# Kernel tuning notes

Measured on AMD Instinct MI355X. Metric: run time of the kernel, lower is better.

Reference implementation:

```python
import jax, jax.numpy as jnp
import numpy as np

N_NODES = 50000
N_EDGES = 800000
D_IN = 256
HID = 128
OUT = 64
NEG_SLOPE = 0.2  # PyG GATConv default leaky_relu slope
EPS = 1e-16      # PyG softmax denominator epsilon


def _gat_conv(x, src, dst, W_src, W_dst, att_src, att_dst, bias, n_nodes):
    """Single-head PyG GATConv with add_self_loops=False.
    Returns (out [N, C_out], alpha [E])."""
    h_src = x @ W_src                     # [N, C]
    h_dst = x @ W_dst                     # [N, C]
    a_src = h_src @ att_src               # [N]
    a_dst = h_dst @ att_dst               # [N]
    logits = jax.nn.leaky_relu(a_src[src] + a_dst[dst], NEG_SLOPE)  # [E]
    # segment softmax over incoming edges of each dst node
    m = jax.ops.segment_max(logits, dst, num_segments=n_nodes)      # [N]
    e = jnp.exp(logits - m[dst])                                    # [E]
    denom = jax.ops.segment_sum(e, dst, num_segments=n_nodes)       # [N]
    alpha = e / (denom[dst] + EPS)                                  # [E]
    msg = h_src[src] * alpha[:, None]                               # [E, C]
    out = jax.ops.segment_sum(msg, dst, num_segments=n_nodes) + bias
    return out, alpha


def setup_inputs() -> dict:
    key = jax.random.key(0)
    ks = jax.random.split(key, 16)
    s = 0.05
    x = jax.random.normal(ks[0], (N_NODES, D_IN), dtype=jnp.float32)
    edge_index = jax.random.randint(ks[1], (2, N_EDGES), 0, N_NODES, dtype=jnp.int64)
    return {
        "x": x,
        "edge_index": edge_index,
        "W_src1": jax.random.normal(ks[2], (D_IN, HID), jnp.float32) * s,
        "W_dst1": jax.random.normal(ks[3], (D_IN, HID), jnp.float32) * s,
        "att_src1": jax.random.normal(ks[4], (HID,), jnp.float32) * s,
        "att_dst1": jax.random.normal(ks[5], (HID,), jnp.float32) * s,
        "b1": jnp.zeros((HID,), jnp.float32),
        "W_lin1": jax.random.normal(ks[6], (D_IN, HID), jnp.float32) * s,
        "b_lin1": jnp.zeros((HID,), jnp.float32),
        "W_src2": jax.random.normal(ks[7], (HID, OUT), jnp.float32) * s,
        "W_dst2": jax.random.normal(ks[8], (HID, OUT), jnp.float32) * s,
        "att_src2": jax.random.normal(ks[9], (OUT,), jnp.float32) * s,
        "att_dst2": jax.random.normal(ks[10], (OUT,), jnp.float32) * s,
        "b2": jnp.zeros((OUT,), jnp.float32),
        "W_lin2": jax.random.normal(ks[11], (HID, OUT), jnp.float32) * s,
        "b_lin2": jnp.zeros((OUT,), jnp.float32),
    }


def reference(x, edge_index, W_src1, W_dst1, att_src1, att_dst1, b1, W_lin1, b_lin1,
              W_src2, W_dst2, att_src2, att_dst2, b2, W_lin2, b_lin2):
    src, dst = edge_index[0], edge_index[1]
    n = x.shape[0]
    h, _ = _gat_conv(x, src, dst, W_src1, W_dst1, att_src1, att_dst1, b1, n)
    h = h + x @ W_lin1 + b_lin1
    h = jax.nn.relu(h)
    out, alpha = _gat_conv(h, src, dst, W_src2, W_dst2, att_src2, att_dst2, b2, n)
    out = out + h @ W_lin2 + b_lin2
    return out, alpha
```

## Files before the change

### kernel.cpp

```cpp
#include <hip/hip_runtime.h>
#include <math.h>

#define D_IN 256
#define HID 128
#define D_OUT 64
#define NEG_SLOPE 0.2f

#define NBUCK 196
#define BCAP  5120
#define P1_EPB 8192

typedef short short8 __attribute__((ext_vector_type(8)));
typedef float floatx4 __attribute__((ext_vector_type(4)));

__device__ __forceinline__ float wave_reduce_sum(float v) {
    #pragma unroll
    for (int off = 32; off > 0; off >>= 1) v += __shfl_xor(v, off, 64);
    return v;
}
__device__ __forceinline__ int wave_scan_incl_i(int v) {
    int lane = threadIdx.x & 63;
    #pragma unroll
    for (int off = 1; off < 64; off <<= 1) {
        int t = __shfl_up(v, off, 64);
        if (lane >= off) v += t;
    }
    return v;
}

__device__ __forceinline__ short f2bf(float f) {
    unsigned u = __float_as_uint(f);
    u += 0x7fffu + ((u >> 16) & 1u);
    return (short)(u >> 16);
}
__device__ __forceinline__ unsigned pk2(float a, float b) {
    return (unsigned)(unsigned short)f2bf(a) | ((unsigned)(unsigned short)f2bf(b) << 16);
}
__device__ __forceinline__ float bflo(unsigned p) { return __uint_as_float(p << 16); }
__device__ __forceinline__ float bfhi(unsigned p) { return __uint_as_float(p & 0xffff0000u); }

__device__ void prep_body(const float* Wsrc1, const float* att_src1,
                          const float* Wdst1, const float* att_dst1,
                          const float* Wsrc2, const float* att_src2,
                          const float* Wdst2, const float* att_dst2,
                          const float* b1, const float* b_lin1,
                          const float* b2, const float* b_lin2,
                          float* v_src1, float* v_dst1, float* v_src2, float* v_dst2,
                          float* bsum1, float* bsum2) {
    int t = threadIdx.x;
    if (t < D_IN) {
        float s1 = 0.f, s2 = 0.f;
        for (int c = 0; c < HID; c++) {
            s1 += Wsrc1[t * HID + c] * att_src1[c];
            s2 += Wdst1[t * HID + c] * att_dst1[c];
        }
        v_src1[t] = s1; v_dst1[t] = s2;
    }
    if (t < HID) {
        float s1 = 0.f, s2 = 0.f;
        for (int c = 0; c < D_OUT; c++) {
            s1 += Wsrc2[t * D_OUT + c] * att_src2[c];
            s2 += Wdst2[t * D_OUT + c] * att_dst2[c];
        }
        v_src2[t] = s1; v_dst2[t] = s2;
        bsum1[t] = b1[t] + b_lin1[t];
    }
    if (t < D_OUT) bsum2[t] = b2[t] + b_lin2[t];
}

__device__ void pack_body(const float* Wa, const float* Wb, short* Wp,
                          int NTG, int NH, int total, int idx) {
    if (idx >= total) return;
    int j = idx & 7;
    int lane = (idx >> 3) & 63;
    int r = idx >> 9;
    int nt = r % NTG;
    int s = r / NTG;
    int k = s * 32 + ((lane >> 4) * 8) + j;
    int cg = nt * 16 + (lane & 15);
    const float* W = (cg < NH) ? Wa : Wb;
    int col = (cg < NH) ? cg : cg - NH;
    Wp[idx] = f2bf(W[(size_t)k * NH + col]);
}

__device__ void bucket_scatter_body(const int* __restrict__ src, const int* __restrict__ dst,
                                    int E, int* bcur, unsigned* ebuf, int blk) {
    __shared__ int hist[NBUCK];
    __shared__ int gbase[NBUCK];
    int t = threadIdx.x;
    for (int i = t; i < NBUCK; i += 256) hist[i] = 0;
    __syncthreads();
    int e0 = blk * P1_EPB;
    int e1 = e0 + P1_EPB; if (e1 > E) e1 = E;
    for (int e = e0 + t; e < e1; e += 256)
        atomicAdd(&hist[dst[e] >> 8], 1);
    __syncthreads();
    for (int i = t; i < NBUCK; i += 256) {
        gbase[i] = atomicAdd(&bcur[i], hist[i]);
        hist[i] = 0;
    }
    __syncthreads();
    for (int e = e0 + t; e < e1; e += 256) {
        int d = dst[e];
        int b = d >> 8;
        int slot = atomicAdd(&hist[b], 1);
        int pos = gbase[b] + slot;
        if (pos < BCAP)
            ebuf[(size_t)b * BCAP + pos] = (unsigned)src[e] | ((unsigned)(d & 255) << 16);
    }
}

__device__ void convert_body(const float* __restrict__ X, unsigned short* __restrict__ xb,
                             int Nn, int rb) {
    int row = rb * 4 + (threadIdx.x >> 6);
    int lane = threadIdx.x & 63;
    if (row >= Nn) return;
    float4 v = *(const float4*)(X + (size_t)row * D_IN + lane * 4);
    ushort4 o;
    o.x = (unsigned short)f2bf(v.x); o.y = (unsigned short)f2bf(v.y);
    o.z = (unsigned short)f2bf(v.z); o.w = (unsigned short)f2bf(v.w);
    *(ushort4*)(xb + (size_t)row * D_IN + lane * 4) = o;
}

__global__ void fused_pre(const int* __restrict__ src, const int* __restrict__ dst, int E,
                          int* bcur, unsigned* ebuf, int P1B,
                          const float* W_src1, const float* W_lin1, short* Wp1,
                          const float* W_src2, const float* W_lin2, short* Wp2,
                          const float* att_src1, const float* W_dst1, const float* att_dst1,
                          const float* att_src2, const float* W_dst2, const float* att_dst2,
                          const float* b1, const float* b_lin1,
                          const float* b2, const float* b_lin2,
                          float* v_src1, float* v_dst1, float* v_src2, float* v_dst2,
                          float* bsum1, float* bsum2,
                          const float* __restrict__ X, unsigned short* __restrict__ xb, int Nn) {
    int bid = blockIdx.x;
    if (bid < P1B) {
        bucket_scatter_body(src, dst, E, bcur, ebuf, bid);
    } else if (bid < P1B + 256) {
        pack_body(W_src1, W_lin1, Wp1, 16, HID, 8 * 16 * 512, (bid - P1B) * 256 + threadIdx.x);
    } else if (bid < P1B + 320) {
        pack_body(W_src2, W_lin2, Wp2, 8, D_OUT, 4 * 8 * 512, (bid - P1B - 256) * 256 + threadIdx.x);
    } else if (bid < P1B + 321) {
        prep_body(W_src1, att_src1, W_dst1, att_dst1, W_src2, att_src2, W_dst2, att_dst2,
                  b1, b_lin1, b2, b_lin2, v_src1, v_dst1, v_src2, v_dst2, bsum1, bsum2);
    } else {
        convert_body(X, xb, Nn, bid - (P1B + 321));
    }
}

__device__ void build_csr_body(const int* __restrict__ bcur, const unsigned* __restrict__ ebuf,
                               int* __restrict__ ssrc, int* __restrict__ row_beg,
                               int* __restrict__ row_end, int Nn, int b) {
    __shared__ int cnt[256];
    __shared__ int ofs[256];
    __shared__ int wsum[4];
    int t = threadIdx.x;
    cnt[t] = 0;
    __syncthreads();
    int n = bcur[b]; if (n > BCAP) n = BCAP;
    const unsigned* eb = ebuf + (size_t)b * BCAP;
    for (int i = t; i < n; i += 256)
        atomicAdd(&cnt[eb[i] >> 16], 1);
    __syncthreads();
    int v = cnt[t];
    int incl = wave_scan_incl_i(v);
    if ((t & 63) == 63) wsum[t >> 6] = incl;
    __syncthreads();
    int add = 0;
    #pragma unroll
    for (int w = 0; w < 4; w++) if (w < (t >> 6)) add += wsum[w];
    int excl = add + incl - v;
    int base = b * BCAP;
    int node = b * 256 + t;
    if (node < Nn) { row_beg[node] = base + excl; row_end[node] = base + excl + v; }
    ofs[t] = base + excl;
    __syncthreads();
    for (int i = t; i < n; i += 256) {
        unsigned r = eb[i];
        int pos = atomicAdd(&ofs[r >> 16], 1);
        ssrc[pos] = (int)(r & 0xffffu);
    }
}

__device__ void dots_body(const unsigned short* __restrict__ xb,
                          const float* __restrict__ vsrc, const float* __restrict__ vdst,
                          float* __restrict__ a_src, float* __restrict__ a_dst,
                          int Nn, int rb) {
    int row = rb * 4 + (threadIdx.x >> 6);
    int lane = threadIdx.x & 63;
    if (row >= Nn) return;
    uint2 p = *(const uint2*)(xb + (size_t)row * D_IN + lane * 4);
    float4 vs = *(const float4*)(vsrc + lane * 4);
    float4 vd = *(const float4*)(vdst + lane * 4);
    float x0 = bflo(p.x), x1 = bfhi(p.x), x2 = bflo(p.y), x3 = bfhi(p.y);
    float ps = x0 * vs.x + x1 * vs.y + x2 * vs.z + x3 * vs.w;
    float pd = x0 * vd.x + x1 * vd.y + x2 * vd.z + x3 * vd.w;
    ps = wave_reduce_sum(ps);
    pd = wave_reduce_sum(pd);
    if (lane == 0) { a_src[row] = ps; a_dst[row] = pd; }
}

template <int KS, int NT>
__device__ void gemm_body(const unsigned short* __restrict__ A,
                          const short* __restrict__ Wp,
                          const float* __restrict__ bias,
                          unsigned short* __restrict__ outb,
                          unsigned short* __restrict__ outc, int M, int bm) {
    const int K = KS * 32;
    const int NTG = 4 * NT;
    const int NH = NT * 32;
    int tid = threadIdx.x;
    int wave = tid >> 6, lane = tid & 63;
    int mr = lane & 15, quad = lane >> 4;

    floatx4 acc[4][NT];
    #pragma unroll
    for (int i = 0; i < 4; i++)
        #pragma unroll
        for (int j = 0; j < NT; j++) acc[i][j] = (floatx4){0.f, 0.f, 0.f, 0.f};

    const unsigned short* arow[4];
    #pragma unroll
    for (int tm = 0; tm < 4; tm++) {
        int gr = bm + tm * 16 + mr;
        if (gr >= M) gr = M - 1;
        arow[tm] = A + (size_t)gr * K + quad * 8;
    }
    const short* bbase = Wp + ((size_t)(wave * NT) * 64 + lane) * 8;

    #pragma unroll
    for (int s = 0; s < KS; s++) {
        short8 af[4], bf[NT];
        #pragma unroll
        for (int tm = 0; tm < 4; tm++)
            af[tm] = *(const short8*)(arow[tm] + s * 32);
        #pragma unroll
        for (int tn = 0; tn < NT; tn++)
            bf[tn] = *(const short8*)(bbase + ((size_t)s * NTG + tn) * 512);
        #pragma unroll
        for (int tn = 0; tn < NT; tn++)
            #pragma unroll
            for (int tm = 0; tm < 4; tm++)
                acc[tm][tn] = __builtin_amdgcn_mfma_f32_16x16x32_bf16(af[tm], bf[tn],
                                                                      acc[tm][tn], 0, 0, 0);
    }

    #pragma unroll
    for (int tm = 0; tm < 4; tm++) {
        #pragma unroll
        for (int tn = 0; tn < NT; tn++) {
            int cg = wave * NT * 16 + tn * 16 + mr;
            if (cg < NH) {
                #pragma unroll
                for (int r = 0; r < 4; r++) {
                    int gr = bm + tm * 16 + quad * 4 + r;
                    if (gr < M)
                        outb[(size_t)gr * NH + cg] = (unsigned short)f2bf(acc[tm][tn][r]);
                }
            } else {
                float bv = bias[cg - NH];
                #pragma unroll
                for (int r = 0; r < 4; r++) {
                    int gr = bm + tm * 16 + quad * 4 + r;
                    if (gr < M)
                        outc[(size_t)gr * NH + (cg - NH)] = (unsigned short)f2bf(acc[tm][tn][r] + bv);
                }
            }
        }
    }
}

__global__ __launch_bounds__(256, 3) void fused_g1(const unsigned short* __restrict__ xb,
                                                   const short* __restrict__ Wp1,
                                                   const float* __restrict__ bsum1,
                                                   unsigned short* __restrict__ h1b,
                                                   unsigned short* __restrict__ lin1b,
                                                   int M, int MB,
                                                   const int* __restrict__ bcur,
                                                   const unsigned* __restrict__ ebuf,
                                                   int* ssrc, int* row_beg, int* row_end, int Nn,
                                                   const float* __restrict__ v_src1,
                                                   const float* __restrict__ v_dst1,
                                                   float* a_src1, float* a_dst1) {
    int bid = blockIdx.x;
    if (bid < MB) {
        gemm_body<8, 4>(xb, Wp1, bsum1, h1b, lin1b, M, bid * 64);
    } else if (bid < MB + NBUCK) {
        build_csr_body(bcur, ebuf, ssrc, row_beg, row_end, Nn, bid - MB);
    } else {
        dots_body(xb, v_src1, v_dst1, a_src1, a_dst1, Nn, bid - MB - NBUCK);
    }
}

template <int KS, int NT>
__global__ __launch_bounds__(256, 3) void gemm_direct(const unsigned short* __restrict__ A,
                                                      const short* __restrict__ Wp,
                                                      const float* __restrict__ bias,
                                                      unsigned short* __restrict__ outb,
                                                      unsigned short* __restrict__ outc, int M) {
    gemm_body<KS, NT>(A, Wp, bias, outb, outc, M, blockIdx.x * 64);
}

__global__ void agg1_kernel(const int* __restrict__ row_beg, const int* __restrict__ row_end,
                            const int* __restrict__ ssrc,
                            const float* __restrict__ a_src, const float* __restrict__ a_dst,
                            const unsigned short* __restrict__ h1b,
                            const unsigned short* __restrict__ linb,
                            const float* __restrict__ vs2, const float* __restrict__ vd2,
                            unsigned short* __restrict__ hb,
                            float* __restrict__ a_src2, float* __restrict__ a_dst2, int Nn) {
    int node = blockIdx.x * 4 + (threadIdx.x >> 6);
    int lane = threadIdx.x & 63;
    if (node >= Nn) return;
    int beg = row_beg[node], end = row_end[node];
    float ad = a_dst[node];

    int qh = lane >> 4, cl = lane & 15;
    float acc[8] = {0.f, 0.f, 0.f, 0.f, 0.f, 0.f, 0.f, 0.f};
    float dsum = 0.f;
    const unsigned short* hcol = h1b + cl * 8;
    int j = beg + qh;
    for (; j + 4 < end; j += 8) {
        int s0 = ssrc[j], s1 = ssrc[j + 4];
        float l0 = a_src[s0] + ad; l0 = (l0 > 0.f) ? l0 : NEG_SLOPE * l0;
        float l1 = a_src[s1] + ad; l1 = (l1 > 0.f) ? l1 : NEG_SLOPE * l1;
        float w0 = __expf(l0), w1 = __expf(l1);
        uint4 p0 = *(const uint4*)(hcol + (size_t)s0 * HID);
        uint4 p1 = *(const uint4*)(hcol + (size_t)s1 * HID);
        acc[0] += w0 * bflo(p0.x); acc[1] += w0 * bfhi(p0.x);
        acc[2] += w0 * bflo(p0.y); acc[3] += w0 * bfhi(p0.y);
        acc[4] += w0 * bflo(p0.z); acc[5] += w0 * bfhi(p0.z);
        acc[6] += w0 * bflo(p0.w); acc[7] += w0 * bfhi(p0.w);
        acc[0] += w1 * bflo(p1.x); acc[1] += w1 * bfhi(p1.x);
        acc[2] += w1 * bflo(p1.y); acc[3] += w1 * bfhi(p1.y);
        acc[4] += w1 * bflo(p1.z); acc[5] += w1 * bfhi(p1.z);
        acc[6] += w1 * bflo(p1.w); acc[7] += w1 * bfhi(p1.w);
        if (cl == 0) dsum += w0 + w1;
    }
    for (; j < end; j += 4) {
        int s0 = ssrc[j];
        float l = a_src[s0] + ad; l = (l > 0.f) ? l : NEG_SLOPE * l;
        float w = __expf(l);
        uint4 p = *(const uint4*)(hcol + (size_t)s0 * HID);
        acc[0] += w * bflo(p.x); acc[1] += w * bfhi(p.x);
        acc[2] += w * bflo(p.y); acc[3] += w * bfhi(p.y);
        acc[4] += w * bflo(p.z); acc[5] += w * bfhi(p.z);
        acc[6] += w * bflo(p.w); acc[7] += w * bfhi(p.w);
        if (cl == 0) dsum += w;
    }
    #pragma unroll
    for (int i = 0; i < 8; i++) {
        acc[i] += __shfl_xor(acc[i], 16, 64);
        acc[i] += __shfl_xor(acc[i], 32, 64);
    }
    dsum = wave_reduce_sum(dsum);
    float inv = 1.f / (dsum + 1e-16f);

    int c = cl * 8;
    uint4 lb = *(const uint4*)(linb + (size_t)node * HID + c);
    float o[8];
    o[0] = fmaxf(acc[0] * inv + bflo(lb.x), 0.f);
    o[1] = fmaxf(acc[1] * inv + bfhi(lb.x), 0.f);
    o[2] = fmaxf(acc[2] * inv + bflo(lb.y), 0.f);
    o[3] = fmaxf(acc[3] * inv + bfhi(lb.y), 0.f);
    o[4] = fmaxf(acc[4] * inv + bflo(lb.z), 0.f);
    o[5] = fmaxf(acc[5] * inv + bfhi(lb.z), 0.f);
    o[6] = fmaxf(acc[6] * inv + bflo(lb.w), 0.f);
    o[7] = fmaxf(acc[7] * inv + bfhi(lb.w), 0.f);
    if (qh == 0) {
        uint4 pk;
        pk.x = pk2(o[0], o[1]); pk.y = pk2(o[2], o[3]);
        pk.z = pk2(o[4], o[5]); pk.w = pk2(o[6], o[7]);
        *(uint4*)&hb[(size_t)node * HID + c] = pk;
    }
    float ps = 0.f, pd = 0.f;
    #pragma unroll
    for (int i = 0; i < 8; i++) { ps += o[i] * vs2[c + i]; pd += o[i] * vd2[c + i]; }
    ps = wave_reduce_sum(ps) * 0.25f;
    pd = wave_reduce_sum(pd) * 0.25f;
    if (lane == 0) { a_src2[node] = ps; a_dst2[node] = pd; }
}

__global__ void agg2_kernel(const int* __restrict__ row_beg, const int* __restrict__ row_end,
                            const int* __restrict__ ssrc,
                            const float* __restrict__ a_src, const float* __restrict__ a_dst,
                            const unsigned short* __restrict__ h2b,
                            const unsigned short* __restrict__ lin2b,
                            float* __restrict__ out, float* __restrict__ sminv, int Nn) {
    int node = blockIdx.x * 4 + (threadIdx.x >> 6);
    int lane = threadIdx.x & 63;
    if (node >= Nn) return;
    int beg = row_beg[node], end = row_end[node];
    float ad = a_dst[node];

    int oh = lane >> 3, cl = lane & 7;
    float acc[8] = {0.f, 0.f, 0.f, 0.f, 0.f, 0.f, 0.f, 0.f};
    float dsum = 0.f;
    const unsigned short* hcol = h2b + cl * 8;
    int j = beg + oh;
    for (; j + 8 < end; j += 16) {
        int s0 = ssrc[j], s1 = ssrc[j + 8];
        float l0 = a_src[s0] + ad; l0 = (l0 > 0.f) ? l0 : NEG_SLOPE * l0;
        float l1 = a_src[s1] + ad; l1 = (l1 > 0.f) ? l1 : NEG_SLOPE * l1;
        float w0 = __expf(l0), w1 = __expf(l1);
        uint4 p0 = *(const uint4*)(hcol + (size_t)s0 * D_OUT);
        uint4 p1 = *(const uint4*)(hcol + (size_t)s1 * D_OUT);
        acc[0] += w0 * bflo(p0.x); acc[1] += w0 * bfhi(p0.x);
        acc[2] += w0 * bflo(p0.y); acc[3] += w0 * bfhi(p0.y);
        acc[4] += w0 * bflo(p0.z); acc[5] += w0 * bfhi(p0.z);
        acc[6] += w0 * bflo(p0.w); acc[7] += w0 * bfhi(p0.w);
        acc[0] += w1 * bflo(p1.x); acc[1] += w1 * bfhi(p1.x);
        acc[2] += w1 * bflo(p1.y); acc[3] += w1 * bfhi(p1.y);
        acc[4] += w1 * bflo(p1.z); acc[5] += w1 * bfhi(p1.z);
        acc[6] += w1 * bflo(p1.w); acc[7] += w1 * bfhi(p1.w);
        if (cl == 0) dsum += w0 + w1;
    }
    for (; j < end; j += 8) {
        int s0 = ssrc[j];
        float l = a_src[s0] + ad; l = (l > 0.f) ? l : NEG_SLOPE * l;
        float w = __expf(l);
        uint4 p = *(const uint4*)(hcol + (size_t)s0 * D_OUT);
        acc[0] += w * bflo(p.x); acc[1] += w * bfhi(p.x);
        acc[2] += w * bflo(p.y); acc[3] += w * bfhi(p.y);
        acc[4] += w * bflo(p.z); acc[5] += w * bfhi(p.z);
        acc[6] += w * bflo(p.w); acc[7] += w * bfhi(p.w);
        if (cl == 0) dsum += w;
    }
    #pragma unroll
    for (int i = 0; i < 8; i++) {
        acc[i] += __shfl_xor(acc[i], 8, 64);
        acc[i] += __shfl_xor(acc[i], 16, 64);
        acc[i] += __shfl_xor(acc[i], 32, 64);
    }
    dsum = wave_reduce_sum(dsum);
    float inv = 1.f / (dsum + 1e-16f);
    if (lane == 0) sminv[node] = inv;

    if (oh == 0) {
        int c = cl * 8;
        uint4 lb = *(const uint4*)(lin2b + (size_t)node * D_OUT + c);
        float4 oa = make_float4(acc[0] * inv + bflo(lb.x), acc[1] * inv + bfhi(lb.x),
                                acc[2] * inv + bflo(lb.y), acc[3] * inv + bfhi(lb.y));
        float4 ob = make_float4(acc[4] * inv + bflo(lb.z), acc[5] * inv + bfhi(lb.z),
                                acc[6] * inv + bflo(lb.w), acc[7] * inv + bfhi(lb.w));
        *(float4*)&out[(size_t)node * D_OUT + c] = oa;
        *(float4*)&out[(size_t)node * D_OUT + c + 4] = ob;
    }
}

__global__ void alpha_kernel(const int* __restrict__ src, const int* __restrict__ dst,
                             const float* __restrict__ a_src2, const float* __restrict__ a_dst2,
                             const float* __restrict__ sminv, float* __restrict__ alpha, int E) {
    int e = blockIdx.x * 256 + threadIdx.x;
    if (e >= E) return;
    int s = src[e], d = dst[e];
    float l = a_src2[s] + a_dst2[d];
    l = (l > 0.f) ? l : NEG_SLOPE * l;
    alpha[e] = __expf(l) * sminv[d];
}

extern "C" void kernel_launch(void* const* d_in, const int* in_sizes, int n_in,
                              void* d_out, int out_size, void* d_ws, size_t ws_size,
                              hipStream_t stream) {
    const float* x        = (const float*)d_in[0];
    const int*   ei       = (const int*)d_in[1];
    const float* W_src1   = (const float*)d_in[2];
    const float* W_dst1   = (const float*)d_in[3];
    const float* att_src1 = (const float*)d_in[4];
    const float* att_dst1 = (const float*)d_in[5];
    const float* b1       = (const float*)d_in[6];
    const float* W_lin1   = (const float*)d_in[7];
    const float* b_lin1   = (const float*)d_in[8];
    const float* W_src2   = (const float*)d_in[9];
    const float* W_dst2   = (const float*)d_in[10];
    const float* att_src2 = (const float*)d_in[11];
    const float* att_dst2 = (const float*)d_in[12];
    const float* b2       = (const float*)d_in[13];
    const float* W_lin2   = (const float*)d_in[14];
    const float* b_lin2   = (const float*)d_in[15];

    const int Nn = in_sizes[0] / D_IN;
    const int E  = in_sizes[1] / 2;
    const int* src = ei;
    const int* dst = ei + E;

    char* w = (char*)d_ws;
    auto alloc = [&](size_t bytes) { char* p = w; w += (bytes + 255) & ~(size_t)255; return p; };
    unsigned short* xb   = (unsigned short*)alloc((size_t)Nn * D_IN * 2);
    unsigned short* h1b  = (unsigned short*)alloc((size_t)Nn * HID * 2);
    unsigned short* lin1b= (unsigned short*)alloc((size_t)Nn * HID * 2);
    unsigned short* hb   = (unsigned short*)alloc((size_t)Nn * HID * 2);
    unsigned short* h2b  = (unsigned short*)alloc((size_t)Nn * D_OUT * 2);
    unsigned short* lin2b= (unsigned short*)alloc((size_t)Nn * D_OUT * 2);
    float* a_src1 = (float*)alloc((size_t)Nn * 4);
    float* a_dst1 = (float*)alloc((size_t)Nn * 4);
    float* a_src2 = (float*)alloc((size_t)Nn * 4);
    float* a_dst2 = (float*)alloc((size_t)Nn * 4);
    float* sminv  = (float*)alloc((size_t)Nn * 4);
    int*   row_beg= (int*)alloc((size_t)Nn * 4);
    int*   row_end= (int*)alloc((size_t)Nn * 4);
    int*   bcur   = (int*)alloc((size_t)NBUCK * 4);
    unsigned* ebuf= (unsigned*)alloc((size_t)NBUCK * BCAP * 4);
    int*   ssrc   = (int*)alloc((size_t)NBUCK * BCAP * 4);
    short* Wp1    = (short*)alloc((size_t)8 * 16 * 512 * 2);
    short* Wp2    = (short*)alloc((size_t)4 * 8 * 512 * 2);
    float* v_src1 = (float*)alloc(D_IN * 4);
    float* v_dst1 = (float*)alloc(D_IN * 4);
    float* v_src2 = (float*)alloc(HID * 4);
    float* v_dst2 = (float*)alloc(HID * 4);
    float* bsum1  = (float*)alloc(HID * 4);
    float* bsum2  = (float*)alloc(D_OUT * 4);

    float* out       = (float*)d_out;
    float* alpha_out = out + (size_t)Nn * D_OUT;

    hipMemsetAsync(bcur, 0, (size_t)NBUCK * 4, stream);

    int P1B = (E + P1_EPB - 1) / P1_EPB;
    int ablocks = (Nn + 3) / 4;
    fused_pre<<<P1B + 321 + ablocks, 256, 0, stream>>>(src, dst, E, bcur, ebuf, P1B,
                                             W_src1, W_lin1, Wp1, W_src2, W_lin2, Wp2,
                                             att_src1, W_dst1, att_dst1,
                                             att_src2, W_dst2, att_dst2,
                                             b1, b_lin1, b2, b_lin2,
                                             v_src1, v_dst1, v_src2, v_dst2, bsum1, bsum2,
                                             x, xb, Nn);

    int mblocks = (Nn + 63) / 64;
    fused_g1<<<mblocks + NBUCK + ablocks, 256, 0, stream>>>(xb, Wp1, bsum1, h1b, lin1b, Nn,
                                                            mblocks, bcur, ebuf, ssrc,
                                                            row_beg, row_end, Nn,
                                                            v_src1, v_dst1, a_src1, a_dst1);

    agg1_kernel<<<ablocks, 256, 0, stream>>>(row_beg, row_end, ssrc, a_src1, a_dst1, h1b, lin1b,
                                             v_src2, v_dst2, hb, a_src2, a_dst2, Nn);

    gemm_direct<4, 2><<<mblocks, 256, 0, stream>>>(hb, Wp2, bsum2, h2b, lin2b, Nn);
    agg2_kernel<<<ablocks, 256, 0, stream>>>(row_beg, row_end, ssrc, a_src2, a_dst2, h2b, lin2b,
                                             out, sminv, Nn);
    int eblocks = (E + 255) / 256;
    alpha_kernel<<<eblocks, 256, 0, stream>>>(src, dst, a_src2, a_dst2, sminv, alpha_out, E);
}
```

Baseline: 275.5 us.

## Split CSR build into finer sub-buckets interleaved with GEMM blocks

```diff
diff --git a/kernel.cpp b/kernel.cpp
--- a/kernel.cpp
+++ b/kernel.cpp
@@ -6,9 +6,11 @@
 #define D_OUT 64
 #define NEG_SLOPE 0.2f
 
-#define NBUCK 196
-#define BCAP  5120
-#define P1_EPB 8192
+#define NBUCK 392
+#define BCAP  2560
+#define NSUB  784
+#define SCAP  1280
+#define P1_EPB 2048
 
 typedef short short8 __attribute__((ext_vector_type(8)));
 typedef float floatx4 __attribute__((ext_vector_type(4)));
@@ -93,7 +95,7 @@
     int e0 = blk * P1_EPB;
     int e1 = e0 + P1_EPB; if (e1 > E) e1 = E;
     for (int e = e0 + t; e < e1; e += 256)
-        atomicAdd(&hist[dst[e] >> 8], 1);
+        atomicAdd(&hist[dst[e] >> 7], 1);
     __syncthreads();
     for (int i = t; i < NBUCK; i += 256) {
         gbase[i] = atomicAdd(&bcur[i], hist[i]);
@@ -102,11 +104,11 @@
     __syncthreads();
     for (int e = e0 + t; e < e1; e += 256) {
         int d = dst[e];
-        int b = d >> 8;
+        int b = d >> 7;
         int slot = atomicAdd(&hist[b], 1);
         int pos = gbase[b] + slot;
         if (pos < BCAP)
-            ebuf[(size_t)b * BCAP + pos] = (unsigned)src[e] | ((unsigned)(d & 255) << 16);
+            ebuf[(size_t)b * BCAP + pos] = (unsigned)src[e] | ((unsigned)(d & 127) << 16);
     }
 }
 
@@ -150,35 +152,37 @@
 
 __device__ void build_csr_body(const int* __restrict__ bcur, const unsigned* __restrict__ ebuf,
                                int* __restrict__ ssrc, int* __restrict__ row_beg,
-                               int* __restrict__ row_end, int Nn, int b) {
-    __shared__ int cnt[256];
-    __shared__ int ofs[256];
-    __shared__ int wsum[4];
+                               int* __restrict__ row_end, int Nn, int g) {
+    __shared__ int cnt[64];
+    __shared__ int ofs[64];
     int t = threadIdx.x;
-    cnt[t] = 0;
+    int B = g >> 1, s = g & 1;
+    if (t < 64) cnt[t] = 0;
     __syncthreads();
-    int n = bcur[b]; if (n > BCAP) n = BCAP;
-    const unsigned* eb = ebuf + (size_t)b * BCAP;
-    for (int i = t; i < n; i += 256)
-        atomicAdd(&cnt[eb[i] >> 16], 1);
+    int n = bcur[B]; if (n > BCAP) n = BCAP;
+    const unsigned* eb = ebuf + (size_t)B * BCAP;
+    for (int i = t; i < n; i += 256) {
+        int loc = eb[i] >> 16;
+        if ((loc >> 6) == s) atomicAdd(&cnt[loc & 63], 1);
+    }
     __syncthreads();
-    int v = cnt[t];
-    int incl = wave_scan_incl_i(v);
-    if ((t & 63) == 63) wsum[t >> 6] = incl;
-    __syncthreads();
-    int add = 0;
-    #pragma unroll
-    for (int w = 0; w < 4; w++) if (w < (t >> 6)) add += wsum[w];
-    int excl = add + incl - v;
-    int base = b * BCAP;
-    int node = b * 256 + t;
-    if (node < Nn) { row_beg[node] = base + excl; row_end[node] = base + excl + v; }
-    ofs[t] = base + excl;
+    int base = g * SCAP;
+    if (t < 64) {
+        int v = cnt[t];
+        int incl = wave_scan_incl_i(v);
+        int excl = incl - v;
+        int node = g * 64 + t;
+        if (node < Nn) { row_beg[node] = base + excl; row_end[node] = base + excl + v; }
+        ofs[t] = base + excl;
+    }
     __syncthreads();
     for (int i = t; i < n; i += 256) {
         unsigned r = eb[i];
-        int pos = atomicAdd(&ofs[r >> 16], 1);
-        ssrc[pos] = (int)(r & 0xffffu);
+        int loc = r >> 16;
+        if ((loc >> 6) == s) {
+            int pos = atomicAdd(&ofs[loc & 63], 1);
+            ssrc[pos] = (int)(r & 0xffffu);
+        }
     }
 }
 
@@ -283,12 +287,17 @@
                                                    const float* __restrict__ v_dst1,
                                                    float* a_src1, float* a_dst1) {
     int bid = blockIdx.x;
-    if (bid < MB) {
-        gemm_body<8, 4>(xb, Wp1, bsum1, h1b, lin1b, M, bid * 64);
-    } else if (bid < MB + NBUCK) {
-        build_csr_body(bcur, ebuf, ssrc, row_beg, row_end, Nn, bid - MB);
+    int NI = 2 * MB;
+    if (bid < NI) {
+        if ((bid & 1) == 0) {
+            gemm_body<8, 4>(xb, Wp1, bsum1, h1b, lin1b, M, (bid >> 1) * 64);
+        } else {
+            int g = bid >> 1;
+            if (g < NSUB)
+                build_csr_body(bcur, ebuf, ssrc, row_beg, row_end, Nn, g);
+        }
     } else {
-        dots_body(xb, v_src1, v_dst1, a_src1, a_dst1, Nn, bid - MB - NBUCK);
+        dots_body(xb, v_src1, v_dst1, a_src1, a_dst1, Nn, bid - NI);
     }
 }
 
@@ -501,7 +510,7 @@
     int*   row_end= (int*)alloc((size_t)Nn * 4);
     int*   bcur   = (int*)alloc((size_t)NBUCK * 4);
     unsigned* ebuf= (unsigned*)alloc((size_t)NBUCK * BCAP * 4);
-    int*   ssrc   = (int*)alloc((size_t)NBUCK * BCAP * 4);
+    int*   ssrc   = (int*)alloc((size_t)NSUB * SCAP * 4);
     short* Wp1    = (short*)alloc((size_t)8 * 16 * 512 * 2);
     short* Wp2    = (short*)alloc((size_t)4 * 8 * 512 * 2);
     float* v_src1 = (float*)alloc(D_IN * 4);
@@ -527,10 +536,10 @@
                                              x, xb, Nn);
 
     int mblocks = (Nn + 63) / 64;
-    fused_g1<<<mblocks + NBUCK + ablocks, 256, 0, stream>>>(xb, Wp1, bsum1, h1b, lin1b, Nn,
-                                                            mblocks, bcur, ebuf, ssrc,
-                                                            row_beg, row_end, Nn,
-                                                            v_src1, v_dst1, a_src1, a_dst1);
+    fused_g1<<<2 * mblocks + ablocks, 256, 0, stream>>>(xb, Wp1, bsum1, h1b, lin1b, Nn,
+                                                        mblocks, bcur, ebuf, ssrc,
+                                                        row_beg, row_end, Nn,
+                                                        v_src1, v_dst1, a_src1, a_dst1);
 
     agg1_kernel<<<ablocks, 256, 0, stream>>>(row_beg, row_end, ssrc, a_src1, a_dst1, h1b, lin1b,
                                              v_src2, v_dst2, hb, a_src2, a_dst2, Nn);
```

Measured after the change: 298.0 us. +8.2%, slower.
